# Optimization experiments

Hardware: AMD Instinct MI355X
Metric: run time of the kernel (lower is better)

The kernel has to match this reference:

```python
import jax, jax.numpy as jnp
import numpy as np

L = 3          # num_layers
H = 128        # hidden_dim
NH = 4         # num heads
DH = H // NH   # head dim
B = 32         # graphs per batch
N = 1024       # nodes per graph
NTOT = B * N
DEG = 16
E = NTOT * DEG
BN_EPS = 1e-5


def setup_inputs() -> dict:
    key = jax.random.key(0)
    ks = jax.random.split(key, 16)
    s = 1.0 / np.sqrt(H)
    inp = {
        "x": jax.random.normal(ks[0], (NTOT, H), jnp.float32),
        "edge_attr": jax.random.normal(ks[1], (E, H), jnp.float32),
        "gine_w1": jax.random.normal(ks[2], (L, H, H), jnp.float32) * s,
        "gine_b1": jnp.zeros((L, H), jnp.float32),
        "gine_bn_g": jnp.ones((L, H), jnp.float32),
        "gine_bn_b": jnp.zeros((L, H), jnp.float32),
        "gine_w2": jax.random.normal(ks[3], (L, H, H), jnp.float32) * s,
        "gine_b2": jnp.zeros((L, H), jnp.float32),
        "attn_wqkv": jax.random.normal(ks[4], (L, 3 * H, H), jnp.float32) * s,
        "attn_bqkv": jnp.zeros((L, 3 * H), jnp.float32),
        "attn_wo": jax.random.normal(ks[5], (L, H, H), jnp.float32) * s,
        "attn_bo": jnp.zeros((L, H), jnp.float32),
        "norm1_g": jnp.ones((L, H), jnp.float32),
        "norm1_b": jnp.zeros((L, H), jnp.float32),
        "norm2_g": jnp.ones((L, H), jnp.float32),
        "norm2_b": jnp.zeros((L, H), jnp.float32),
        "norm3_g": jnp.ones((L, H), jnp.float32),
        "norm3_b": jnp.zeros((L, H), jnp.float32),
        "mlp_w1": jax.random.normal(ks[6], (L, 2 * H, H), jnp.float32) * s,
        "mlp_b1": jnp.zeros((L, 2 * H), jnp.float32),
        "mlp_w2": jax.random.normal(ks[7], (L, H, 2 * H), jnp.float32) * (1.0 / np.sqrt(2 * H)),
        "mlp_b2": jnp.zeros((L, H), jnp.float32),
    }
    # intra-graph random edges: local src/dst in [0, N) plus per-graph offset
    offs = (jnp.arange(E, dtype=jnp.int32) // (N * DEG)) * N  # graph offset per edge
    src = jax.random.randint(ks[8], (E,), 0, N, jnp.int32) + offs
    dst = jax.random.randint(ks[9], (E,), 0, N, jnp.int32) + offs
    inp["edge_index"] = jnp.stack([src, dst]).astype(jnp.int32)
    inp["batch"] = (jnp.arange(NTOT, dtype=jnp.int32) // N)
    return inp


def _bn(x, g, b):
    m = x.mean(axis=0)
    v = jnp.var(x, axis=0)
    return (x - m) * jax.lax.rsqrt(v + BN_EPS) * g + b


def _gps_forward(x, edge_attr, gine_w1, gine_b1, gine_bn_g, gine_bn_b, gine_w2, gine_b2,
                 attn_wqkv, attn_bqkv, attn_wo, attn_bo,
                 norm1_g, norm1_b, norm2_g, norm2_b, norm3_g, norm3_b,
                 mlp_w1, mlp_b1, mlp_w2, mlp_b2, edge_index, batch):
    src, dst = edge_index[0], edge_index[1]
    for i in range(L):
        # ---- GINEConv: msg = relu(x_j + e), sum-scatter, nn-MLP on x + aggr (eps=0)
        msg = jax.nn.relu(x[src] + edge_attr)                       # [E, H]
        aggr = jax.ops.segment_sum(msg, dst, num_segments=NTOT)     # [NTOT, H]
        h = x + aggr
        h = h @ gine_w1[i].T + gine_b1[i]
        h = jax.nn.relu(_bn(h, gine_bn_g[i], gine_bn_b[i]))
        h = h @ gine_w2[i].T + gine_b2[i]
        h_local = _bn(h + x, norm1_g[i], norm1_b[i])                # residual + norm1
        # ---- global multi-head attention on x (dense per-graph, equal sizes)
        xb = x.reshape(B, N, H)
        qkv = xb @ attn_wqkv[i].T + attn_bqkv[i]                    # [B, N, 3H]
        q, k, v = jnp.split(qkv, 3, axis=-1)
        q = q.reshape(B, N, NH, DH).transpose(0, 2, 1, 3)           # [B, nh, N, dh]
        k = k.reshape(B, N, NH, DH).transpose(0, 2, 1, 3)
        v = v.reshape(B, N, NH, DH).transpose(0, 2, 1, 3)
        scores = jnp.einsum("bhqd,bhkd->bhqk", q, k) / np.sqrt(DH)
        attn = jax.nn.softmax(scores, axis=-1)
        o = jnp.einsum("bhqk,bhkd->bhqd", attn, v)
        o = o.transpose(0, 2, 1, 3).reshape(B, N, H) @ attn_wo[i].T + attn_bo[i]
        h_attn = _bn(o.reshape(NTOT, H) + x, norm2_g[i], norm2_b[i])
        # ---- combine + FFN + norm3
        out = h_local + h_attn
        ff = jax.nn.relu(out @ mlp_w1[i].T + mlp_b1[i]) @ mlp_w2[i].T + mlp_b2[i]
        x = _bn(out + ff, norm3_g[i], norm3_b[i])
        if i != L - 1:
            x = jax.nn.relu(x)
    return x


def reference(x, edge_attr, gine_w1, gine_b1, gine_bn_g, gine_bn_b, gine_w2, gine_b2,
              attn_wqkv, attn_bqkv, attn_wo, attn_bo,
              norm1_g, norm1_b, norm2_g, norm2_b, norm3_g, norm3_b,
              mlp_w1, mlp_b1, mlp_w2, mlp_b2, edge_index, batch):
    return _gps_forward(x, edge_attr, gine_w1, gine_b1, gine_bn_g, gine_bn_b, gine_w2, gine_b2,
                        attn_wqkv, attn_bqkv, attn_wo, attn_bo,
                        norm1_g, norm1_b, norm2_g, norm2_b, norm3_g, norm3_b,
                        mlp_w1, mlp_b1, mlp_w2, mlp_b2, edge_index, batch)
```

## Files before the change

kernel.cpp:

```cpp
#include <hip/hip_runtime.h>
#include <hip/hip_bf16.h>
#include <math.h>

#define NTOT 32768
#define HDIM 128
#define NE   524288
#define NGRAPH 32
#define NNODE 1024
#define NHEAD 4
#define DHEAD 32

typedef __attribute__((ext_vector_type(8))) short bf8v;
typedef __attribute__((ext_vector_type(4))) float f4v;

__device__ __forceinline__ float4 ld4(const float* p){ return *(const float4*)p; }

__device__ __forceinline__ unsigned short bf16rn(float f){
  union { float f; unsigned u; } x; x.f = f;
  unsigned r = x.u + 0x7FFF + ((x.u >> 16) & 1);
  return (unsigned short)(r >> 16);
}
__device__ __forceinline__ unsigned pk2(float a, float b){
  unsigned r;
  asm("v_cvt_pk_bf16_f32 %0, %1, %2" : "=v"(r) : "v"(a), "v"(b));
  return r;
}
__device__ __forceinline__ float bf2f(unsigned short u){
  union { unsigned u; float f; } x; x.u = ((unsigned)u) << 16;
  return x.f;
}

__global__ void k_count(const int* __restrict__ dst, int* __restrict__ deg){
  int e = blockIdx.x*256 + threadIdx.x;
  atomicAdd(&deg[dst[e]], 1);
}

__global__ __launch_bounds__(1024) void k_scan(const int* __restrict__ deg,
                                               int* __restrict__ indptr,
                                               int* __restrict__ cursor){
  __shared__ int sm[1024];
  int t = threadIdx.x;
  int base = t*32;
  int s = 0;
  for (int j=0;j<32;j++) s += deg[base+j];
  sm[t] = s; __syncthreads();
  for (int off=1; off<1024; off<<=1){
    int v = (t>=off) ? sm[t-off] : 0;
    __syncthreads();
    sm[t] += v;
    __syncthreads();
  }
  int ex = sm[t] - s;
  for (int j=0;j<32;j++){
    int d = deg[base+j];
    indptr[base+j] = ex; cursor[base+j] = ex;
    ex += d;
  }
  if (t == 1023) indptr[NTOT] = ex;
}

__global__ void k_fill(const int* __restrict__ dst, int* __restrict__ cursor,
                       int* __restrict__ perm){
  int e = blockIdx.x*256 + threadIdx.x;
  int pos = atomicAdd(&cursor[dst[e]], 1);
  perm[pos] = e;
}

__global__ __launch_bounds__(256) void k_eaprep(const float* __restrict__ ea,
    const int* __restrict__ src, const int* __restrict__ perm,
    unsigned short* __restrict__ EAb, int* __restrict__ SRCp){
  int tid = threadIdx.x;
  int p = blockIdx.x*8 + (tid>>5);
  int c4 = (tid&31)*4;
  int e = perm[p];
  float4 v = ld4(&ea[(size_t)e*HDIM + c4]);
  uint2 o; o.x = pk2(v.x, v.y); o.y = pk2(v.z, v.w);
  *(uint2*)&EAb[(size_t)p*HDIM + c4] = o;
  if ((tid&31) == 0) SRCp[p] = src[e];
}

__global__ __launch_bounds__(256) void k_aggr(const float* __restrict__ x,
                       const unsigned short* __restrict__ EAb,
                       const int* __restrict__ SRCp, const int* __restrict__ indptr,
                       float* __restrict__ aggr){
  int tid = threadIdx.x;
  int n = blockIdx.x*8 + (tid>>5);
  int c4 = (tid&31)*4;
  int p0 = indptr[n], p1 = indptr[n+1];
  float4 acc = make_float4(0.f,0.f,0.f,0.f);
  for (int p=p0;p<p1;p++){
    int s = SRCp[p];
    uint2 ev = *(const uint2*)&EAb[(size_t)p*HDIM + c4];
    float4 xv = ld4(&x[(size_t)s*HDIM + c4]);
    acc.x += fmaxf(xv.x + bf2f((unsigned short)(ev.x & 0xffff)), 0.f);
    acc.y += fmaxf(xv.y + bf2f((unsigned short)(ev.x >> 16)), 0.f);
    acc.z += fmaxf(xv.z + bf2f((unsigned short)(ev.y & 0xffff)), 0.f);
    acc.w += fmaxf(xv.w + bf2f((unsigned short)(ev.y >> 16)), 0.f);
  }
  *(float4*)&aggr[(size_t)n*HDIM + c4] = acc;
}

template<bool ADDA, bool BNA, bool RELU, bool EP, bool STATS>
__global__ __launch_bounds__(256) void k_gemm16(const float* __restrict__ A,
    const float* __restrict__ A2, const float* __restrict__ bnst,
    const float* __restrict__ W, const float* __restrict__ bias,
    const float* __restrict__ Ep, float* __restrict__ C, float* __restrict__ slot,
    int N, int K){
  __shared__ uint4 Asm[128*4];
  __shared__ uint4 Wsm[128*4];
  __shared__ float sred[256];
  int tid = threadIdx.x;
  int w = tid>>6, l = tid&63;
  int q = l&15, g = l>>4;
  int m0 = blockIdx.x*128, n0 = blockIdx.y*128;
  int wr = (w>>1)*64, wc = (w&1)*64;
  f4v acc[4][4];
  #pragma unroll
  for (int i=0;i<4;i++)
    #pragma unroll
    for (int j=0;j<4;j++) acc[i][j] = (f4v){0.f,0.f,0.f,0.f};
  int srow = tid & 127;
  int sgh  = tid >> 7;
  int sswz = (srow>>1)&3;

  for (int kc=0; kc<K; kc+=32){
    const float* pa = &A[(size_t)(m0+srow)*K + kc + sgh*16];
    float4 v0=ld4(pa), v1=ld4(pa+4), v2=ld4(pa+8), v3=ld4(pa+12);
    if (ADDA){
      const float* pb = &A2[(size_t)(m0+srow)*K + kc + sgh*16];
      float4 u0=ld4(pb), u1=ld4(pb+4), u2=ld4(pb+8), u3=ld4(pb+12);
      v0.x+=u0.x; v0.y+=u0.y; v0.z+=u0.z; v0.w+=u0.w;
      v1.x+=u1.x; v1.y+=u1.y; v1.z+=u1.z; v1.w+=u1.w;
      v2.x+=u2.x; v2.y+=u2.y; v2.z+=u2.z; v2.w+=u2.w;
      v3.x+=u3.x; v3.y+=u3.y; v3.z+=u3.z; v3.w+=u3.w;
    }
    if (BNA){
      int kb = kc + sgh*16;
      float4 s0=ld4(&bnst[256+kb]),  s1=ld4(&bnst[256+kb+4]);
      float4 s2=ld4(&bnst[256+kb+8]),s3=ld4(&bnst[256+kb+12]);
      float4 h0=ld4(&bnst[384+kb]),  h1=ld4(&bnst[384+kb+4]);
      float4 h2=ld4(&bnst[384+kb+8]),h3=ld4(&bnst[384+kb+12]);
      v0.x=fmaxf(v0.x*s0.x+h0.x,0.f); v0.y=fmaxf(v0.y*s0.y+h0.y,0.f);
      v0.z=fmaxf(v0.z*s0.z+h0.z,0.f); v0.w=fmaxf(v0.w*s0.w+h0.w,0.f);
      v1.x=fmaxf(v1.x*s1.x+h1.x,0.f); v1.y=fmaxf(v1.y*s1.y+h1.y,0.f);
      v1.z=fmaxf(v1.z*s1.z+h1.z,0.f); v1.w=fmaxf(v1.w*s1.w+h1.w,0.f);
      v2.x=fmaxf(v2.x*s2.x+h2.x,0.f); v2.y=fmaxf(v2.y*s2.y+h2.y,0.f);
      v2.z=fmaxf(v2.z*s2.z+h2.z,0.f); v2.w=fmaxf(v2.w*s2.w+h2.w,0.f);
      v3.x=fmaxf(v3.x*s3.x+h3.x,0.f); v3.y=fmaxf(v3.y*s3.y+h3.y,0.f);
      v3.z=fmaxf(v3.z*s3.z+h3.z,0.f); v3.w=fmaxf(v3.w*s3.w+h3.w,0.f);
    }
    uint4 ca, cb;
    ca.x=pk2(v0.x,v0.y); ca.y=pk2(v0.z,v0.w); ca.z=pk2(v1.x,v1.y); ca.w=pk2(v1.z,v1.w);
    cb.x=pk2(v2.x,v2.y); cb.y=pk2(v2.z,v2.w); cb.z=pk2(v3.x,v3.y); cb.w=pk2(v3.z,v3.w);
    const float* pw = &W[(size_t)(n0+srow)*K + kc + sgh*16];
    float4 w0=ld4(pw), w1=ld4(pw+4), w2=ld4(pw+8), w3=ld4(pw+12);
    uint4 da, db;
    da.x=pk2(w0.x,w0.y); da.y=pk2(w0.z,w0.w); da.z=pk2(w1.x,w1.y); da.w=pk2(w1.z,w1.w);
    db.x=pk2(w2.x,w2.y); db.y=pk2(w2.z,w2.w); db.z=pk2(w3.x,w3.y); db.w=pk2(w3.z,w3.w);
    __syncthreads();
    Asm[srow*4 + ((2*sgh  )^sswz)] = ca;
    Asm[srow*4 + ((2*sgh+1)^sswz)] = cb;
    Wsm[srow*4 + ((2*sgh  )^sswz)] = da;
    Wsm[srow*4 + ((2*sgh+1)^sswz)] = db;
    __syncthreads();
    bf8v af[4], bfv[4];
    #pragma unroll
    for (int mt=0;mt<4;mt++){
      int R = wr + 16*mt + q;
      af[mt] = *(const bf8v*)&Asm[R*4 + (g ^ ((R>>1)&3))];
    }
    #pragma unroll
    for (int nt=0;nt<4;nt++){
      int R = wc + 16*nt + q;
      bfv[nt] = *(const bf8v*)&Wsm[R*4 + (g ^ ((R>>1)&3))];
    }
    #pragma unroll
    for (int mt=0;mt<4;mt++)
      #pragma unroll
      for (int nt=0;nt<4;nt++)
        acc[mt][nt] = __builtin_amdgcn_mfma_f32_16x16x32_bf16(af[mt], bfv[nt], acc[mt][nt], 0,0,0);
  }
  float bbv[4];
  #pragma unroll
  for (int nt=0;nt<4;nt++) bbv[nt] = bias[n0 + wc + 16*nt + q];
  float csum[4] = {0.f,0.f,0.f,0.f}, csq[4] = {0.f,0.f,0.f,0.f};
  #pragma unroll
  for (int mt=0;mt<4;mt++){
    int row0 = m0 + wr + 16*mt + 4*g;
    #pragma unroll
    for (int nt=0;nt<4;nt++){
      int col = n0 + wc + 16*nt + q;
      #pragma unroll
      for (int r=0;r<4;r++){
        size_t off = (size_t)(row0+r)*N + col;
        float v = acc[mt][nt][r] + bbv[nt];
        if (EP) v += Ep[off];
        if (RELU) v = fmaxf(v, 0.f);
        C[off] = v;
        if (STATS){ csum[nt] += v; csq[nt] += v*v; }
      }
    }
  }
  if (STATS){
    if (tid < 128){ sred[tid] = 0.f; sred[128+tid] = 0.f; }
    __syncthreads();
    #pragma unroll
    for (int nt=0;nt<4;nt++){
      int col = wc + 16*nt + q;
      atomicAdd(&sred[col], csum[nt]);
      atomicAdd(&sred[128+col], csq[nt]);
    }
    __syncthreads();
    if (tid < 128){
      atomicAdd(&slot[tid], sred[tid]);
      atomicAdd(&slot[128+tid], sred[128+tid]);
    }
  }
}

__global__ __launch_bounds__(256) void k_gemmqkv(const float* __restrict__ A,
    const float* __restrict__ W, const float* __restrict__ bias,
    unsigned short* __restrict__ Qb, unsigned short* __restrict__ Kb,
    unsigned short* __restrict__ VT){
  __shared__ uint4 Asm[128*4];
  __shared__ uint4 Wsm[128*4];
  __shared__ unsigned short Sm[128*136];
  int tid = threadIdx.x;
  int w = tid>>6, l = tid&63;
  int q = l&15, g = l>>4;
  int which = blockIdx.y;
  int m0 = blockIdx.x*128, n0 = which*128;
  int wr = (w>>1)*64, wc = (w&1)*64;
  const int K = 128;
  f4v acc[4][4];
  #pragma unroll
  for (int i=0;i<4;i++)
    #pragma unroll
    for (int j=0;j<4;j++) acc[i][j] = (f4v){0.f,0.f,0.f,0.f};
  int srow = tid & 127;
  int sgh  = tid >> 7;
  int sswz = (srow>>1)&3;
  for (int kc=0; kc<K; kc+=32){
    const float* pa = &A[(size_t)(m0+srow)*K + kc + sgh*16];
    float4 v0=ld4(pa), v1=ld4(pa+4), v2=ld4(pa+8), v3=ld4(pa+12);
    uint4 ca, cb;
    ca.x=pk2(v0.x,v0.y); ca.y=pk2(v0.z,v0.w); ca.z=pk2(v1.x,v1.y); ca.w=pk2(v1.z,v1.w);
    cb.x=pk2(v2.x,v2.y); cb.y=pk2(v2.z,v2.w); cb.z=pk2(v3.x,v3.y); cb.w=pk2(v3.z,v3.w);
    const float* pw = &W[(size_t)(n0+srow)*K + kc + sgh*16];
    float4 w0=ld4(pw), w1=ld4(pw+4), w2=ld4(pw+8), w3=ld4(pw+12);
    uint4 da, db;
    da.x=pk2(w0.x,w0.y); da.y=pk2(w0.z,w0.w); da.z=pk2(w1.x,w1.y); da.w=pk2(w1.z,w1.w);
    db.x=pk2(w2.x,w2.y); db.y=pk2(w2.z,w2.w); db.z=pk2(w3.x,w3.y); db.w=pk2(w3.z,w3.w);
    __syncthreads();
    Asm[srow*4 + ((2*sgh  )^sswz)] = ca;
    Asm[srow*4 + ((2*sgh+1)^sswz)] = cb;
    Wsm[srow*4 + ((2*sgh  )^sswz)] = da;
    Wsm[srow*4 + ((2*sgh+1)^sswz)] = db;
    __syncthreads();
    bf8v af[4], bfv[4];
    #pragma unroll
    for (int mt=0;mt<4;mt++){
      int R = wr + 16*mt + q;
      af[mt] = *(const bf8v*)&Asm[R*4 + (g ^ ((R>>1)&3))];
    }
    #pragma unroll
    for (int nt=0;nt<4;nt++){
      int R = wc + 16*nt + q;
      bfv[nt] = *(const bf8v*)&Wsm[R*4 + (g ^ ((R>>1)&3))];
    }
    #pragma unroll
    for (int mt=0;mt<4;mt++)
      #pragma unroll
      for (int nt=0;nt<4;nt++)
        acc[mt][nt] = __builtin_amdgcn_mfma_f32_16x16x32_bf16(af[mt], bfv[nt], acc[mt][nt], 0,0,0);
  }
  const float QSC = 0.17677669529663687f * 1.4426950408889634f;
  float scale = (which==0) ? QSC : 1.0f;
  float bbv[4];
  #pragma unroll
  for (int nt=0;nt<4;nt++) bbv[nt] = bias[n0 + wc + 16*nt + q];
  __syncthreads();
  if (which < 2){
    #pragma unroll
    for (int mt=0;mt<4;mt++){
      int row0 = wr + 16*mt + 4*g;
      #pragma unroll
      for (int nt=0;nt<4;nt++){
        int col = wc + 16*nt + q;
        #pragma unroll
        for (int r=0;r<4;r++)
          Sm[(row0+r)*136 + col] = bf16rn((acc[mt][nt][r] + bbv[nt]) * scale);
      }
    }
    __syncthreads();
    unsigned short* dst = (which==0) ? Qb : Kb;
    #pragma unroll
    for (int it=0; it<8; it++){
      int idx = tid + it*256;
      int row = idx >> 4, c8 = (idx & 15) * 8;
      uint4 v = *(const uint4*)&Sm[row*136 + c8];
      *(uint4*)&dst[(size_t)(m0+row)*128 + c8] = v;
    }
  } else {
    #pragma unroll
    for (int mt=0;mt<4;mt++){
      int row0 = wr + 16*mt + 4*g;
      #pragma unroll
      for (int nt=0;nt<4;nt++){
        int col = wc + 16*nt + q;
        uint2 p;
        p.x = pk2(acc[mt][nt][0] + bbv[nt], acc[mt][nt][1] + bbv[nt]);
        p.y = pk2(acc[mt][nt][2] + bbv[nt], acc[mt][nt][3] + bbv[nt]);
        *(uint2*)&Sm[col*136 + row0] = p;
      }
    }
    __syncthreads();
    int gg = m0 >> 10;
    int nl0 = m0 - gg*1024;
    #pragma unroll
    for (int it=0; it<8; it++){
      int idx = tid + it*256;
      int c = idx >> 4, n8 = (idx & 15) * 8;
      uint4 v = *(const uint4*)&Sm[c*136 + n8];
      *(uint4*)&VT[((size_t)gg*128 + c)*1024 + nl0 + n8] = v;
    }
  }
}

__global__ __launch_bounds__(128) void k_bnfinal(const float* __restrict__ g, const float* __restrict__ b,
                                                 float* __restrict__ slot){
  int f = threadIdx.x;
  const float invn = 1.0f/32768.0f;
  float mean = slot[f]*invn;
  float var  = slot[128+f]*invn - mean*mean;
  float sc = g[f] * rsqrtf(var + 1e-5f);
  slot[256+f] = sc;
  slot[384+f] = b[f] - mean*sc;
}

template<bool RELU>
__global__ __launch_bounds__(256) void k_bnapply(const float* __restrict__ X,
                                                 const float* __restrict__ slot,
                                                 float* __restrict__ Y){
  size_t i = (size_t)blockIdx.x*256 + threadIdx.x;
  int c = (int)(i & 31) * 4;
  float4 v = ((const float4*)X)[i];
  float4 sc = *(const float4*)&slot[256+c];
  float4 sh = *(const float4*)&slot[384+c];
  float4 y;
  y.x = v.x*sc.x + sh.x; y.y = v.y*sc.y + sh.y;
  y.z = v.z*sc.z + sh.z; y.w = v.w*sc.w + sh.w;
  if (RELU){
    y.x=fmaxf(y.x,0.f); y.y=fmaxf(y.y,0.f); y.z=fmaxf(y.z,0.f); y.w=fmaxf(y.w,0.f);
  }
  ((float4*)Y)[i] = y;
}

__global__ __launch_bounds__(256) void k_add2bn(const float* __restrict__ A, const float* __restrict__ s1,
                                                const float* __restrict__ B, const float* __restrict__ s2,
                                                float* __restrict__ C){
  size_t i = (size_t)blockIdx.x*256 + threadIdx.x;
  int c = (int)(i & 31) * 4;
  float4 a = ((const float4*)A)[i];
  float4 b = ((const float4*)B)[i];
  float4 c1 = *(const float4*)&s1[256+c], d1 = *(const float4*)&s1[384+c];
  float4 c2 = *(const float4*)&s2[256+c], d2 = *(const float4*)&s2[384+c];
  float4 y;
  y.x = a.x*c1.x+d1.x + b.x*c2.x+d2.x;
  y.y = a.y*c1.y+d1.y + b.y*c2.y+d2.y;
  y.z = a.z*c1.z+d1.z + b.z*c2.z+d2.z;
  y.w = a.w*c1.w+d1.w + b.w*c2.w+d2.w;
  ((float4*)C)[i] = y;
}

__global__ __launch_bounds__(256) void k_flash2(const unsigned short* __restrict__ Qb,
    const unsigned short* __restrict__ Kb, const unsigned short* __restrict__ VT,
    float* __restrict__ O){
  __shared__ unsigned short Pl[4][16*72];
  int tid = threadIdx.x;
  int w = tid >> 6, l = tid & 63;
  int q = l & 15, grp = l >> 4;
  int qt = blockIdx.x, h = blockIdx.y, g = blockIdx.z;
  size_t gbase = (size_t)g*1024;
  size_t qrow0 = gbase + qt*64 + w*16;
  const unsigned short* Vp = VT + ((size_t)(g*4 + h)*32)*1024;
  bf8v qf = *(const bf8v*)&Qb[(qrow0 + q)*128 + h*32 + 8*grp];
  unsigned short* Pw = &Pl[w][0];
  float m = -1e30f, lsum = 0.f;
  f4v o0 = {0.f,0.f,0.f,0.f}, o1 = {0.f,0.f,0.f,0.f};
  for (int kt=0; kt<16; kt++){
    int k0 = kt*64;
    f4v st[4];
    #pragma unroll
    for (int t=0;t<4;t++){
      bf8v kf = *(const bf8v*)&Kb[(gbase + k0 + 16*t + q)*128 + h*32 + 8*grp];
      st[t] = __builtin_amdgcn_mfma_f32_16x16x32_bf16(kf, qf, (f4v){0.f,0.f,0.f,0.f}, 0,0,0);
    }
    float smax = st[0][0];
    #pragma unroll
    for (int t=0;t<4;t++)
      #pragma unroll
      for (int r=0;r<4;r++) smax = fmaxf(smax, st[t][r]);
    smax = fmaxf(smax, __shfl_xor(smax, 16));
    smax = fmaxf(smax, __shfl_xor(smax, 32));
    float mnew = fmaxf(m, smax);
    float alpha = exp2f(m - mnew);
    float psum = 0.f;
    #pragma unroll
    for (int t=0;t<4;t++){
      float p0 = exp2f(st[t][0]-mnew), p1 = exp2f(st[t][1]-mnew);
      float p2 = exp2f(st[t][2]-mnew), p3 = exp2f(st[t][3]-mnew);
      psum += (p0+p1)+(p2+p3);
      *(unsigned*)&Pw[q*72 + 16*t + 4*grp]     = pk2(p0,p1);
      *(unsigned*)&Pw[q*72 + 16*t + 4*grp + 2] = pk2(p2,p3);
    }
    psum += __shfl_xor(psum, 16);
    psum += __shfl_xor(psum, 32);
    lsum = lsum*alpha + psum;
    m = mnew;
    f4v aD;
    #pragma unroll
    for (int r=0;r<4;r++) aD[r] = __shfl(alpha, 4*grp + r);
    #pragma unroll
    for (int r=0;r<4;r++){ o0[r] *= aD[r]; o1[r] *= aD[r]; }
    bf8v pa0 = *(const bf8v*)&Pw[q*72 + 8*grp];
    bf8v pa1 = *(const bf8v*)&Pw[q*72 + 32 + 8*grp];
    bf8v v00 = *(const bf8v*)&Vp[(size_t)q*1024      + k0 + 8*grp];
    bf8v v01 = *(const bf8v*)&Vp[(size_t)q*1024      + k0 + 32 + 8*grp];
    bf8v v10 = *(const bf8v*)&Vp[(size_t)(16+q)*1024 + k0 + 8*grp];
    bf8v v11 = *(const bf8v*)&Vp[(size_t)(16+q)*1024 + k0 + 32 + 8*grp];
    o0 = __builtin_amdgcn_mfma_f32_16x16x32_bf16(pa0, v00, o0, 0,0,0);
    o0 = __builtin_amdgcn_mfma_f32_16x16x32_bf16(pa1, v01, o0, 0,0,0);
    o1 = __builtin_amdgcn_mfma_f32_16x16x32_bf16(pa0, v10, o1, 0,0,0);
    o1 = __builtin_amdgcn_mfma_f32_16x16x32_bf16(pa1, v11, o1, 0,0,0);
  }
  f4v lD;
  #pragma unroll
  for (int r=0;r<4;r++) lD[r] = __shfl(lsum, 4*grp + r);
  #pragma unroll
  for (int r=0;r<4;r++){
    float inv = 1.0f/lD[r];
    size_t row = qrow0 + 4*grp + r;
    O[row*HDIM + h*32 + q]      = o0[r]*inv;
    O[row*HDIM + h*32 + 16 + q] = o1[r]*inv;
  }
}

extern "C" void kernel_launch(void* const* d_in, const int* in_sizes, int n_in,
                              void* d_out, int out_size, void* d_ws, size_t ws_size,
                              hipStream_t stream){
  const float* x_in      = (const float*)d_in[0];
  const float* edge_attr = (const float*)d_in[1];
  const float* gine_w1   = (const float*)d_in[2];
  const float* gine_b1   = (const float*)d_in[3];
  const float* gine_bn_g = (const float*)d_in[4];
  const float* gine_bn_b = (const float*)d_in[5];
  const float* gine_w2   = (const float*)d_in[6];
  const float* gine_b2   = (const float*)d_in[7];
  const float* attn_wqkv = (const float*)d_in[8];
  const float* attn_bqkv = (const float*)d_in[9];
  const float* attn_wo   = (const float*)d_in[10];
  const float* attn_bo   = (const float*)d_in[11];
  const float* norm1_g   = (const float*)d_in[12];
  const float* norm1_b   = (const float*)d_in[13];
  const float* norm2_g   = (const float*)d_in[14];
  const float* norm2_b   = (const float*)d_in[15];
  const float* norm3_g   = (const float*)d_in[16];
  const float* norm3_b   = (const float*)d_in[17];
  const float* mlp_w1    = (const float*)d_in[18];
  const float* mlp_b1    = (const float*)d_in[19];
  const float* mlp_w2    = (const float*)d_in[20];
  const float* mlp_b2    = (const float*)d_in[21];
  const int* edge_index  = (const int*)d_in[22];
  const int* srcp = edge_index;
  const int* dstp = edge_index + NE;
  float* out = (float*)d_out;

  float* ws = (float*)d_ws;
  const size_t U = 4194304;
  float* X     = ws;
  float* AGGR  = ws + 1*U;
  float* H1    = ws + 2*U;
  float* H2    = ws + 3*U;
  float* OUT   = ws + 4*U;
  float* FF    = ws + 5*U;
  unsigned short* Qb  = (unsigned short*)(ws + 7*U);
  unsigned short* Kb  = Qb + (size_t)NTOT*128;
  unsigned short* VTb = Kb + (size_t)NTOT*128;
  float* STATS = ws + 10*U;
  int* IW      = (int*)(STATS + 12*512);
  int* deg     = IW;
  int* indptr  = IW + 32768;
  int* cursor  = IW + 32768 + 32772;
  int* perm    = cursor + 32768;
  unsigned short* EAb = (unsigned short*)(ws + 13*U);
  int* SRCp    = (int*)(ws + 21*U + U/2);

  hipMemsetAsync(STATS, 0, 12*512*sizeof(float), stream);
  hipMemsetAsync(deg, 0, NTOT*sizeof(int), stream);
  k_count<<<NE/256, 256, 0, stream>>>(dstp, deg);
  k_scan<<<1, 1024, 0, stream>>>(deg, indptr, cursor);
  k_fill<<<NE/256, 256, 0, stream>>>(dstp, cursor, perm);
  k_eaprep<<<NE/8, 256, 0, stream>>>(edge_attr, srcp, perm, EAb, SRCp);
  hipMemcpyAsync(X, x_in, (size_t)NTOT*HDIM*sizeof(float), hipMemcpyDeviceToDevice, stream);

  const int GAPPLY = (NTOT*HDIM/4)/256;
  dim3 gemmg1(NTOT/128, 1), gemmg2(NTOT/128, 2), gemmqkvg(NTOT/128, 3);

  for (int i=0;i<3;i++){
    const float* W1 = gine_w1 + (size_t)i*HDIM*HDIM;
    const float* B1 = gine_b1 + (size_t)i*HDIM;
    const float* W2 = gine_w2 + (size_t)i*HDIM*HDIM;
    const float* B2 = gine_b2 + (size_t)i*HDIM;
    const float* WQ = attn_wqkv + (size_t)i*3*HDIM*HDIM;
    const float* BQ = attn_bqkv + (size_t)i*3*HDIM;
    const float* WO = attn_wo + (size_t)i*HDIM*HDIM;
    const float* BO = attn_bo + (size_t)i*HDIM;
    const float* WM1 = mlp_w1 + (size_t)i*2*HDIM*HDIM;
    const float* BM1 = mlp_b1 + (size_t)i*2*HDIM;
    const float* WM2 = mlp_w2 + (size_t)i*2*HDIM*HDIM;
    const float* BM2 = mlp_b2 + (size_t)i*HDIM;
    float* S0 = STATS + (size_t)(i*4+0)*512;
    float* S1 = STATS + (size_t)(i*4+1)*512;
    float* S2 = STATS + (size_t)(i*4+2)*512;
    float* S3 = STATS + (size_t)(i*4+3)*512;

    k_aggr<<<NTOT/8, 256, 0, stream>>>(X, EAb, SRCp, indptr, AGGR);
    k_gemm16<true,false,false,false,true><<<gemmg1, 256, 0, stream>>>(X, AGGR, nullptr, W1, B1, nullptr, H1, S0, 128, 128);
    k_bnfinal<<<1, 128, 0, stream>>>(gine_bn_g + (size_t)i*HDIM, gine_bn_b + (size_t)i*HDIM, S0);
    k_gemm16<false,true,false,true,true><<<gemmg1, 256, 0, stream>>>(H1, nullptr, S0, W2, B2, X, AGGR, S1, 128, 128);
    k_bnfinal<<<1, 128, 0, stream>>>(norm1_g + (size_t)i*HDIM, norm1_b + (size_t)i*HDIM, S1);

    k_gemmqkv<<<gemmqkvg, 256, 0, stream>>>(X, WQ, BQ, Qb, Kb, VTb);
    k_flash2<<<dim3(16, NHEAD, NGRAPH), 256, 0, stream>>>(Qb, Kb, VTb, H1);
    k_gemm16<false,false,false,true,true><<<gemmg1, 256, 0, stream>>>(H1, nullptr, nullptr, WO, BO, X, H2, S2, 128, 128);
    k_bnfinal<<<1, 128, 0, stream>>>(norm2_g + (size_t)i*HDIM, norm2_b + (size_t)i*HDIM, S2);

    k_add2bn<<<GAPPLY, 256, 0, stream>>>(AGGR, S1, H2, S2, OUT);
    k_gemm16<false,false,true,false,false><<<gemmg2, 256, 0, stream>>>(OUT, nullptr, nullptr, WM1, BM1, nullptr, FF, nullptr, 256, 128);
    k_gemm16<false,false,false,true,true><<<gemmg1, 256, 0, stream>>>(FF, nullptr, nullptr, WM2, BM2, OUT, H2, S3, 128, 256);
    k_bnfinal<<<1, 128, 0, stream>>>(norm3_g + (size_t)i*HDIM, norm3_b + (size_t)i*HDIM, S3);
    float* dest = (i==2) ? out : X;
    if (i<2) k_bnapply<true ><<<GAPPLY, 256, 0, stream>>>(H2, S3, dest);
    else     k_bnapply<false><<<GAPPLY, 256, 0, stream>>>(H2, S3, dest);
  }
}
```

Before: 1.162 ms.

## Store activations and weights in bf16, drop LDS staging, fuse BN finalize into GEMMs

All intermediate activations (X, hidden, Q/K/V, FF, OUT) now live in bf16 instead of fp32, and weights are pre-converted to bf16 once per call. The GEMMs load MFMA fragments straight from global memory without LDS staging and use 128x64 tiles. BN finalize kernels are removed: scale and shift are computed in the consuming GEMM prologue or the apply kernel, and the add2bn pass is folded into the MLP1 GEMM. This cuts memory traffic and kernel launches, at the cost of extra bf16 rounding of residuals and BN inputs, plus uncoalesced direct global fragment loads.

```diff
diff --git a/kernel.cpp b/kernel.cpp
--- a/kernel.cpp
+++ b/kernel.cpp
@@ -12,20 +12,21 @@
 
 typedef __attribute__((ext_vector_type(8))) short bf8v;
 typedef __attribute__((ext_vector_type(4))) float f4v;
+typedef unsigned short u16;
 
 __device__ __forceinline__ float4 ld4(const float* p){ return *(const float4*)p; }
 
-__device__ __forceinline__ unsigned short bf16rn(float f){
+__device__ __forceinline__ u16 bf16rn(float f){
   union { float f; unsigned u; } x; x.f = f;
   unsigned r = x.u + 0x7FFF + ((x.u >> 16) & 1);
-  return (unsigned short)(r >> 16);
+  return (u16)(r >> 16);
 }
 __device__ __forceinline__ unsigned pk2(float a, float b){
   unsigned r;
   asm("v_cvt_pk_bf16_f32 %0, %1, %2" : "=v"(r) : "v"(a), "v"(b));
   return r;
 }
-__device__ __forceinline__ float bf2f(unsigned short u){
+__device__ __forceinline__ float bf2f(u16 u){
   union { unsigned u; float f; } x; x.u = ((unsigned)u) << 16;
   return x.f;
 }
@@ -68,7 +69,7 @@
 
 __global__ __launch_bounds__(256) void k_eaprep(const float* __restrict__ ea,
     const int* __restrict__ src, const int* __restrict__ perm,
-    unsigned short* __restrict__ EAb, int* __restrict__ SRCp){
+    u16* __restrict__ EAb, int* __restrict__ SRCp){
   int tid = threadIdx.x;
   int p = blockIdx.x*8 + (tid>>5);
   int c4 = (tid&31)*4;
@@ -79,197 +80,191 @@
   if ((tid&31) == 0) SRCp[p] = src[e];
 }
 
-__global__ __launch_bounds__(256) void k_aggr(const float* __restrict__ x,
-                       const unsigned short* __restrict__ EAb,
+__global__ __launch_bounds__(256) void k_xprep(const float* __restrict__ x, u16* __restrict__ Xb){
+  size_t i = ((size_t)blockIdx.x*256 + threadIdx.x)*4;
+  float4 v = ld4(&x[i]);
+  uint2 o; o.x = pk2(v.x,v.y); o.y = pk2(v.z,v.w);
+  *(uint2*)&Xb[i] = o;
+}
+
+__global__ __launch_bounds__(256) void k_wprep(const float* s0,const float* s1,const float* s2,
+    const float* s3,const float* s4,const float* s5, u16* __restrict__ Wb){
+  const float* srcs[6] = {s0,s1,s2,s3,s4,s5};
+  const int cnt4[6] = {12288,12288,36864,12288,24576,24576};
+  const int off[6]  = {0,49152,98304,245760,294912,393216};
+  int y = blockIdx.y;
+  int i = blockIdx.x*256 + threadIdx.x;
+  if (i >= cnt4[y]) return;
+  float4 v = ld4(&srcs[y][(size_t)i*4]);
+  uint2 o; o.x = pk2(v.x,v.y); o.y = pk2(v.z,v.w);
+  *(uint2*)&Wb[off[y] + (size_t)i*4] = o;
+}
+
+__global__ __launch_bounds__(256) void k_aggr(const u16* __restrict__ Xb,
+                       const u16* __restrict__ EAb,
                        const int* __restrict__ SRCp, const int* __restrict__ indptr,
-                       float* __restrict__ aggr){
+                       u16* __restrict__ Hb){
   int tid = threadIdx.x;
   int n = blockIdx.x*8 + (tid>>5);
   int c4 = (tid&31)*4;
   int p0 = indptr[n], p1 = indptr[n+1];
-  float4 acc = make_float4(0.f,0.f,0.f,0.f);
+  float a0=0.f,a1=0.f,a2=0.f,a3=0.f;
   for (int p=p0;p<p1;p++){
     int s = SRCp[p];
+    uint2 xv = *(const uint2*)&Xb[(size_t)s*HDIM + c4];
     uint2 ev = *(const uint2*)&EAb[(size_t)p*HDIM + c4];
-    float4 xv = ld4(&x[(size_t)s*HDIM + c4]);
-    acc.x += fmaxf(xv.x + bf2f((unsigned short)(ev.x & 0xffff)), 0.f);
-    acc.y += fmaxf(xv.y + bf2f((unsigned short)(ev.x >> 16)), 0.f);
-    acc.z += fmaxf(xv.z + bf2f((unsigned short)(ev.y & 0xffff)), 0.f);
-    acc.w += fmaxf(xv.w + bf2f((unsigned short)(ev.y >> 16)), 0.f);
-  }
-  *(float4*)&aggr[(size_t)n*HDIM + c4] = acc;
-}
-
-template<bool ADDA, bool BNA, bool RELU, bool EP, bool STATS>
-__global__ __launch_bounds__(256) void k_gemm16(const float* __restrict__ A,
-    const float* __restrict__ A2, const float* __restrict__ bnst,
-    const float* __restrict__ W, const float* __restrict__ bias,
-    const float* __restrict__ Ep, float* __restrict__ C, float* __restrict__ slot,
-    int N, int K){
-  __shared__ uint4 Asm[128*4];
-  __shared__ uint4 Wsm[128*4];
-  __shared__ float sred[256];
+    a0 += fmaxf(bf2f((u16)(xv.x&0xffff)) + bf2f((u16)(ev.x&0xffff)), 0.f);
+    a1 += fmaxf(bf2f((u16)(xv.x>>16))    + bf2f((u16)(ev.x>>16)), 0.f);
+    a2 += fmaxf(bf2f((u16)(xv.y&0xffff)) + bf2f((u16)(ev.y&0xffff)), 0.f);
+    a3 += fmaxf(bf2f((u16)(xv.y>>16))    + bf2f((u16)(ev.y>>16)), 0.f);
+  }
+  uint2 xn = *(const uint2*)&Xb[(size_t)n*HDIM + c4];
+  a0 += bf2f((u16)(xn.x&0xffff)); a1 += bf2f((u16)(xn.x>>16));
+  a2 += bf2f((u16)(xn.y&0xffff)); a3 += bf2f((u16)(xn.y>>16));
+  uint2 o; o.x = pk2(a0,a1); o.y = pk2(a2,a3);
+  *(uint2*)&Hb[(size_t)n*HDIM + c4] = o;
+}
+
+template<bool BNA, bool DUAL, bool RELU, bool EP, bool STATS, bool WROUT>
+__global__ __launch_bounds__(256) void k_bgemm(const u16* __restrict__ Ab,
+    const u16* __restrict__ A2b,
+    const float* __restrict__ slotA, const float* __restrict__ gA, const float* __restrict__ bA,
+    const float* __restrict__ slotB, const float* __restrict__ gB, const float* __restrict__ bB,
+    const u16* __restrict__ Wb, const float* __restrict__ bias,
+    const u16* __restrict__ Epb, u16* __restrict__ Cb,
+    u16* __restrict__ OUTb, float* __restrict__ slotOut, int N, int K){
+  __shared__ float sbnA[256];
+  __shared__ float sbnB[256];
+  __shared__ float sred[128];
   int tid = threadIdx.x;
   int w = tid>>6, l = tid&63;
   int q = l&15, g = l>>4;
-  int m0 = blockIdx.x*128, n0 = blockIdx.y*128;
-  int wr = (w>>1)*64, wc = (w&1)*64;
-  f4v acc[4][4];
-  #pragma unroll
-  for (int i=0;i<4;i++)
+  int m0 = blockIdx.x*128, n0 = blockIdx.y*64;
+  int wr = w*32;
+  const float invn = 1.0f/32768.0f;
+  if (BNA || DUAL){
+    if (tid < 128){
+      float mean = slotA[tid]*invn;
+      float var  = slotA[128+tid]*invn - mean*mean;
+      float sc = gA[tid] * rsqrtf(var + 1e-5f);
+      sbnA[tid] = sc; sbnA[128+tid] = bA[tid] - mean*sc;
+      if (DUAL){
+        float mean2 = slotB[tid]*invn;
+        float var2  = slotB[128+tid]*invn - mean2*mean2;
+        float sc2 = gB[tid] * rsqrtf(var2 + 1e-5f);
+        sbnB[tid] = sc2; sbnB[128+tid] = bB[tid] - mean2*sc2;
+      }
+    }
+  }
+  if (STATS && tid < 128) sred[tid] = 0.f;
+  if (BNA || DUAL || STATS) __syncthreads();
+
+  f4v acc[2][4];
+  #pragma unroll
+  for (int i=0;i<2;i++)
     #pragma unroll
     for (int j=0;j<4;j++) acc[i][j] = (f4v){0.f,0.f,0.f,0.f};
-  int srow = tid & 127;
-  int sgh  = tid >> 7;
-  int sswz = (srow>>1)&3;
 
   for (int kc=0; kc<K; kc+=32){
-    const float* pa = &A[(size_t)(m0+srow)*K + kc + sgh*16];
-    float4 v0=ld4(pa), v1=ld4(pa+4), v2=ld4(pa+8), v3=ld4(pa+12);
-    if (ADDA){
-      const float* pb = &A2[(size_t)(m0+srow)*K + kc + sgh*16];
-      float4 u0=ld4(pb), u1=ld4(pb+4), u2=ld4(pb+8), u3=ld4(pb+12);
-      v0.x+=u0.x; v0.y+=u0.y; v0.z+=u0.z; v0.w+=u0.w;
-      v1.x+=u1.x; v1.y+=u1.y; v1.z+=u1.z; v1.w+=u1.w;
-      v2.x+=u2.x; v2.y+=u2.y; v2.z+=u2.z; v2.w+=u2.w;
-      v3.x+=u3.x; v3.y+=u3.y; v3.z+=u3.z; v3.w+=u3.w;
-    }
-    if (BNA){
-      int kb = kc + sgh*16;
-      float4 s0=ld4(&bnst[256+kb]),  s1=ld4(&bnst[256+kb+4]);
-      float4 s2=ld4(&bnst[256+kb+8]),s3=ld4(&bnst[256+kb+12]);
-      float4 h0=ld4(&bnst[384+kb]),  h1=ld4(&bnst[384+kb+4]);
-      float4 h2=ld4(&bnst[384+kb+8]),h3=ld4(&bnst[384+kb+12]);
-      v0.x=fmaxf(v0.x*s0.x+h0.x,0.f); v0.y=fmaxf(v0.y*s0.y+h0.y,0.f);
-      v0.z=fmaxf(v0.z*s0.z+h0.z,0.f); v0.w=fmaxf(v0.w*s0.w+h0.w,0.f);
-      v1.x=fmaxf(v1.x*s1.x+h1.x,0.f); v1.y=fmaxf(v1.y*s1.y+h1.y,0.f);
-      v1.z=fmaxf(v1.z*s1.z+h1.z,0.f); v1.w=fmaxf(v1.w*s1.w+h1.w,0.f);
-      v2.x=fmaxf(v2.x*s2.x+h2.x,0.f); v2.y=fmaxf(v2.y*s2.y+h2.y,0.f);
-      v2.z=fmaxf(v2.z*s2.z+h2.z,0.f); v2.w=fmaxf(v2.w*s2.w+h2.w,0.f);
-      v3.x=fmaxf(v3.x*s3.x+h3.x,0.f); v3.y=fmaxf(v3.y*s3.y+h3.y,0.f);
-      v3.z=fmaxf(v3.z*s3.z+h3.z,0.f); v3.w=fmaxf(v3.w*s3.w+h3.w,0.f);
-    }
-    uint4 ca, cb;
-    ca.x=pk2(v0.x,v0.y); ca.y=pk2(v0.z,v0.w); ca.z=pk2(v1.x,v1.y); ca.w=pk2(v1.z,v1.w);
-    cb.x=pk2(v2.x,v2.y); cb.y=pk2(v2.z,v2.w); cb.z=pk2(v3.x,v3.y); cb.w=pk2(v3.z,v3.w);
-    const float* pw = &W[(size_t)(n0+srow)*K + kc + sgh*16];
-    float4 w0=ld4(pw), w1=ld4(pw+4), w2=ld4(pw+8), w3=ld4(pw+12);
-    uint4 da, db;
-    da.x=pk2(w0.x,w0.y); da.y=pk2(w0.z,w0.w); da.z=pk2(w1.x,w1.y); da.w=pk2(w1.z,w1.w);
-    db.x=pk2(w2.x,w2.y); db.y=pk2(w2.z,w2.w); db.z=pk2(w3.x,w3.y); db.w=pk2(w3.z,w3.w);
-    __syncthreads();
-    Asm[srow*4 + ((2*sgh  )^sswz)] = ca;
-    Asm[srow*4 + ((2*sgh+1)^sswz)] = cb;
-    Wsm[srow*4 + ((2*sgh  )^sswz)] = da;
-    Wsm[srow*4 + ((2*sgh+1)^sswz)] = db;
-    __syncthreads();
-    bf8v af[4], bfv[4];
-    #pragma unroll
-    for (int mt=0;mt<4;mt++){
-      int R = wr + 16*mt + q;
-      af[mt] = *(const bf8v*)&Asm[R*4 + (g ^ ((R>>1)&3))];
+    bf8v af[2], bfv[4];
+    #pragma unroll
+    for (int mt=0;mt<2;mt++){
+      int row = m0 + wr + 16*mt + q;
+      if (!BNA && !DUAL){
+        af[mt] = *(const bf8v*)&Ab[(size_t)row*K + kc + 8*g];
+      } else {
+        union { bf8v b; u16 s[8]; unsigned u[4]; } ra, r2, ro;
+        ra.b = *(const bf8v*)&Ab[(size_t)row*K + kc + 8*g];
+        if (DUAL) r2.b = *(const bf8v*)&A2b[(size_t)row*K + kc + 8*g];
+        float v[8];
+        #pragma unroll
+        for (int j=0;j<8;j++){
+          int kk = kc + 8*g + j;
+          float f = bf2f(ra.s[j]) * sbnA[kk] + sbnA[128+kk];
+          if (BNA) f = fmaxf(f, 0.f);
+          if (DUAL) f += bf2f(r2.s[j]) * sbnB[kk] + sbnB[128+kk];
+          v[j] = f;
+        }
+        ro.u[0]=pk2(v[0],v[1]); ro.u[1]=pk2(v[2],v[3]);
+        ro.u[2]=pk2(v[4],v[5]); ro.u[3]=pk2(v[6],v[7]);
+        af[mt] = ro.b;
+        if (WROUT && blockIdx.y == 0)
+          *(uint4*)&OUTb[(size_t)row*K + kc + 8*g] = *(uint4*)ro.u;
+      }
     }
     #pragma unroll
     for (int nt=0;nt<4;nt++){
-      int R = wc + 16*nt + q;
-      bfv[nt] = *(const bf8v*)&Wsm[R*4 + (g ^ ((R>>1)&3))];
-    }
-    #pragma unroll
-    for (int mt=0;mt<4;mt++)
+      int col = n0 + 16*nt + q;
+      bfv[nt] = *(const bf8v*)&Wb[(size_t)col*K + kc + 8*g];
+    }
+    #pragma unroll
+    for (int mt=0;mt<2;mt++)
       #pragma unroll
       for (int nt=0;nt<4;nt++)
         acc[mt][nt] = __builtin_amdgcn_mfma_f32_16x16x32_bf16(af[mt], bfv[nt], acc[mt][nt], 0,0,0);
   }
   float bbv[4];
   #pragma unroll
-  for (int nt=0;nt<4;nt++) bbv[nt] = bias[n0 + wc + 16*nt + q];
+  for (int nt=0;nt<4;nt++) bbv[nt] = bias[n0 + 16*nt + q];
   float csum[4] = {0.f,0.f,0.f,0.f}, csq[4] = {0.f,0.f,0.f,0.f};
   #pragma unroll
-  for (int mt=0;mt<4;mt++){
+  for (int mt=0;mt<2;mt++){
     int row0 = m0 + wr + 16*mt + 4*g;
     #pragma unroll
     for (int nt=0;nt<4;nt++){
-      int col = n0 + wc + 16*nt + q;
+      int col = n0 + 16*nt + q;
       #pragma unroll
       for (int r=0;r<4;r++){
         size_t off = (size_t)(row0+r)*N + col;
         float v = acc[mt][nt][r] + bbv[nt];
-        if (EP) v += Ep[off];
+        if (EP) v += bf2f(Epb[off]);
         if (RELU) v = fmaxf(v, 0.f);
-        C[off] = v;
+        Cb[off] = bf16rn(v);
         if (STATS){ csum[nt] += v; csq[nt] += v*v; }
       }
     }
   }
   if (STATS){
-    if (tid < 128){ sred[tid] = 0.f; sred[128+tid] = 0.f; }
+    #pragma unroll
+    for (int nt=0;nt<4;nt++){
+      int c = 16*nt + q;
+      atomicAdd(&sred[c], csum[nt]);
+      atomicAdd(&sred[64+c], csq[nt]);
+    }
     __syncthreads();
-    #pragma unroll
-    for (int nt=0;nt<4;nt++){
-      int col = wc + 16*nt + q;
-      atomicAdd(&sred[col], csum[nt]);
-      atomicAdd(&sred[128+col], csq[nt]);
-    }
-    __syncthreads();
-    if (tid < 128){
-      atomicAdd(&slot[tid], sred[tid]);
-      atomicAdd(&slot[128+tid], sred[128+tid]);
-    }
-  }
-}
-
-__global__ __launch_bounds__(256) void k_gemmqkv(const float* __restrict__ A,
-    const float* __restrict__ W, const float* __restrict__ bias,
-    unsigned short* __restrict__ Qb, unsigned short* __restrict__ Kb,
-    unsigned short* __restrict__ VT){
-  __shared__ uint4 Asm[128*4];
-  __shared__ uint4 Wsm[128*4];
-  __shared__ unsigned short Sm[128*136];
+    if (tid < 64){
+      atomicAdd(&slotOut[n0+tid], sred[tid]);
+      atomicAdd(&slotOut[128+n0+tid], sred[64+tid]);
+    }
+  }
+}
+
+__global__ __launch_bounds__(256) void k_qkvgemm(const u16* __restrict__ Ab,
+    const u16* __restrict__ Wb, const float* __restrict__ bias,
+    u16* __restrict__ Qb, u16* __restrict__ Kb, u16* __restrict__ VT){
+  __shared__ u16 Sm[128*72];
   int tid = threadIdx.x;
   int w = tid>>6, l = tid&63;
   int q = l&15, g = l>>4;
-  int which = blockIdx.y;
-  int m0 = blockIdx.x*128, n0 = which*128;
-  int wr = (w>>1)*64, wc = (w&1)*64;
+  int m0 = blockIdx.x*128, n0 = blockIdx.y*64;
+  int which = blockIdx.y >> 1, half = blockIdx.y & 1;
+  int wr = w*32;
   const int K = 128;
-  f4v acc[4][4];
-  #pragma unroll
-  for (int i=0;i<4;i++)
+  f4v acc[2][4];
+  #pragma unroll
+  for (int i=0;i<2;i++)
     #pragma unroll
     for (int j=0;j<4;j++) acc[i][j] = (f4v){0.f,0.f,0.f,0.f};
-  int srow = tid & 127;
-  int sgh  = tid >> 7;
-  int sswz = (srow>>1)&3;
   for (int kc=0; kc<K; kc+=32){
-    const float* pa = &A[(size_t)(m0+srow)*K + kc + sgh*16];
-    float4 v0=ld4(pa), v1=ld4(pa+4), v2=ld4(pa+8), v3=ld4(pa+12);
-    uint4 ca, cb;
-    ca.x=pk2(v0.x,v0.y); ca.y=pk2(v0.z,v0.w); ca.z=pk2(v1.x,v1.y); ca.w=pk2(v1.z,v1.w);
-    cb.x=pk2(v2.x,v2.y); cb.y=pk2(v2.z,v2.w); cb.z=pk2(v3.x,v3.y); cb.w=pk2(v3.z,v3.w);
-    const float* pw = &W[(size_t)(n0+srow)*K + kc + sgh*16];
-    float4 w0=ld4(pw), w1=ld4(pw+4), w2=ld4(pw+8), w3=ld4(pw+12);
-    uint4 da, db;
-    da.x=pk2(w0.x,w0.y); da.y=pk2(w0.z,w0.w); da.z=pk2(w1.x,w1.y); da.w=pk2(w1.z,w1.w);
-    db.x=pk2(w2.x,w2.y); db.y=pk2(w2.z,w2.w); db.z=pk2(w3.x,w3.y); db.w=pk2(w3.z,w3.w);
-    __syncthreads();
-    Asm[srow*4 + ((2*sgh  )^sswz)] = ca;
-    Asm[srow*4 + ((2*sgh+1)^sswz)] = cb;
-    Wsm[srow*4 + ((2*sgh  )^sswz)] = da;
-    Wsm[srow*4 + ((2*sgh+1)^sswz)] = db;
-    __syncthreads();
-    bf8v af[4], bfv[4];
-    #pragma unroll
-    for (int mt=0;mt<4;mt++){
-      int R = wr + 16*mt + q;
-      af[mt] = *(const bf8v*)&Asm[R*4 + (g ^ ((R>>1)&3))];
-    }
-    #pragma unroll
-    for (int nt=0;nt<4;nt++){
-      int R = wc + 16*nt + q;
-      bfv[nt] = *(const bf8v*)&Wsm[R*4 + (g ^ ((R>>1)&3))];
-    }
-    #pragma unroll
-    for (int mt=0;mt<4;mt++)
+    bf8v af[2], bfv[4];
+    #pragma unroll
+    for (int mt=0;mt<2;mt++)
+      af[mt] = *(const bf8v*)&Ab[(size_t)(m0+wr+16*mt+q)*K + kc + 8*g];
+    #pragma unroll
+    for (int nt=0;nt<4;nt++)
+      bfv[nt] = *(const bf8v*)&Wb[(size_t)(n0+16*nt+q)*K + kc + 8*g];
+    #pragma unroll
+    for (int mt=0;mt<2;mt++)
       #pragma unroll
       for (int nt=0;nt<4;nt++)
         acc[mt][nt] = __builtin_amdgcn_mfma_f32_16x16x32_bf16(af[mt], bfv[nt], acc[mt][nt], 0,0,0);
@@ -278,114 +273,100 @@
   float scale = (which==0) ? QSC : 1.0f;
   float bbv[4];
   #pragma unroll
-  for (int nt=0;nt<4;nt++) bbv[nt] = bias[n0 + wc + 16*nt + q];
-  __syncthreads();
+  for (int nt=0;nt<4;nt++) bbv[nt] = bias[n0 + 16*nt + q];
   if (which < 2){
     #pragma unroll
-    for (int mt=0;mt<4;mt++){
+    for (int mt=0;mt<2;mt++){
       int row0 = wr + 16*mt + 4*g;
       #pragma unroll
       for (int nt=0;nt<4;nt++){
-        int col = wc + 16*nt + q;
+        int c = 16*nt + q;
         #pragma unroll
         for (int r=0;r<4;r++)
-          Sm[(row0+r)*136 + col] = bf16rn((acc[mt][nt][r] + bbv[nt]) * scale);
+          Sm[(row0+r)*72 + c] = bf16rn((acc[mt][nt][r] + bbv[nt]) * scale);
       }
     }
     __syncthreads();
-    unsigned short* dst = (which==0) ? Qb : Kb;
-    #pragma unroll
-    for (int it=0; it<8; it++){
+    u16* dst = (which==0) ? Qb : Kb;
+    #pragma unroll
+    for (int it=0; it<4; it++){
       int idx = tid + it*256;
-      int row = idx >> 4, c8 = (idx & 15) * 8;
-      uint4 v = *(const uint4*)&Sm[row*136 + c8];
-      *(uint4*)&dst[(size_t)(m0+row)*128 + c8] = v;
+      int row = idx >> 3, c8 = (idx & 7) * 8;
+      uint4 v = *(const uint4*)&Sm[row*72 + c8];
+      *(uint4*)&dst[(size_t)(m0+row)*128 + half*64 + c8] = v;
     }
   } else {
     #pragma unroll
-    for (int mt=0;mt<4;mt++){
+    for (int mt=0;mt<2;mt++){
       int row0 = wr + 16*mt + 4*g;
       #pragma unroll
       for (int nt=0;nt<4;nt++){
-        int col = wc + 16*nt + q;
+        int c = 16*nt + q;
         uint2 p;
         p.x = pk2(acc[mt][nt][0] + bbv[nt], acc[mt][nt][1] + bbv[nt]);
         p.y = pk2(acc[mt][nt][2] + bbv[nt], acc[mt][nt][3] + bbv[nt]);
-        *(uint2*)&Sm[col*136 + row0] = p;
+        *(uint2*)&Sm[c*136 + row0] = p;
       }
     }
     __syncthreads();
     int gg = m0 >> 10;
     int nl0 = m0 - gg*1024;
     #pragma unroll
-    for (int it=0; it<8; it++){
+    for (int it=0; it<4; it++){
       int idx = tid + it*256;
       int c = idx >> 4, n8 = (idx & 15) * 8;
       uint4 v = *(const uint4*)&Sm[c*136 + n8];
-      *(uint4*)&VT[((size_t)gg*128 + c)*1024 + nl0 + n8] = v;
-    }
-  }
-}
-
-__global__ __launch_bounds__(128) void k_bnfinal(const float* __restrict__ g, const float* __restrict__ b,
-                                                 float* __restrict__ slot){
-  int f = threadIdx.x;
+      *(uint4*)&VT[((size_t)gg*128 + half*64 + c)*1024 + nl0 + n8] = v;
+    }
+  }
+}
+
+template<bool RELU, bool F32OUT>
+__global__ __launch_bounds__(256) void k_bnapply(const u16* __restrict__ X,
+    const float* __restrict__ slot, const float* __restrict__ gv, const float* __restrict__ bv,
+    u16* __restrict__ Yb, float* __restrict__ Yf){
+  int idx = blockIdx.x*256 + threadIdx.x;
+  int row = idx >> 4, c8 = (idx & 15) * 8;
   const float invn = 1.0f/32768.0f;
-  float mean = slot[f]*invn;
-  float var  = slot[128+f]*invn - mean*mean;
-  float sc = g[f] * rsqrtf(var + 1e-5f);
-  slot[256+f] = sc;
-  slot[384+f] = b[f] - mean*sc;
-}
-
-template<bool RELU>
-__global__ __launch_bounds__(256) void k_bnapply(const float* __restrict__ X,
-                                                 const float* __restrict__ slot,
-                                                 float* __restrict__ Y){
-  size_t i = (size_t)blockIdx.x*256 + threadIdx.x;
-  int c = (int)(i & 31) * 4;
-  float4 v = ((const float4*)X)[i];
-  float4 sc = *(const float4*)&slot[256+c];
-  float4 sh = *(const float4*)&slot[384+c];
-  float4 y;
-  y.x = v.x*sc.x + sh.x; y.y = v.y*sc.y + sh.y;
-  y.z = v.z*sc.z + sh.z; y.w = v.w*sc.w + sh.w;
-  if (RELU){
-    y.x=fmaxf(y.x,0.f); y.y=fmaxf(y.y,0.f); y.z=fmaxf(y.z,0.f); y.w=fmaxf(y.w,0.f);
-  }
-  ((float4*)Y)[i] = y;
-}
-
-__global__ __launch_bounds__(256) void k_add2bn(const float* __restrict__ A, const float* __restrict__ s1,
-                                                const float* __restrict__ B, const float* __restrict__ s2,
-                                                float* __restrict__ C){
-  size_t i = (size_t)blockIdx.x*256 + threadIdx.x;
-  int c = (int)(i & 31) * 4;
-  float4 a = ((const float4*)A)[i];
-  float4 b = ((const float4*)B)[i];
-  float4 c1 = *(const float4*)&s1[256+c], d1 = *(const float4*)&s1[384+c];
-  float4 c2 = *(const float4*)&s2[256+c], d2 = *(const float4*)&s2[384+c];
-  float4 y;
-  y.x = a.x*c1.x+d1.x + b.x*c2.x+d2.x;
-  y.y = a.y*c1.y+d1.y + b.y*c2.y+d2.y;
-  y.z = a.z*c1.z+d1.z + b.z*c2.z+d2.z;
-  y.w = a.w*c1.w+d1.w + b.w*c2.w+d2.w;
-  ((float4*)C)[i] = y;
-}
-
-__global__ __launch_bounds__(256) void k_flash2(const unsigned short* __restrict__ Qb,
-    const unsigned short* __restrict__ Kb, const unsigned short* __restrict__ VT,
-    float* __restrict__ O){
-  __shared__ unsigned short Pl[4][16*72];
+  union { uint4 u; u16 s[8]; } iv;
+  iv.u = *(const uint4*)&X[(size_t)row*HDIM + c8];
+  float o[8];
+  #pragma unroll
+  for (int j=0;j<8;j++){
+    int c = c8+j;
+    float mean = slot[c]*invn;
+    float var  = slot[128+c]*invn - mean*mean;
+    float sc = gv[c] * rsqrtf(var + 1e-5f);
+    float sh = bv[c] - mean*sc;
+    float v = bf2f(iv.s[j])*sc + sh;
+    if (RELU) v = fmaxf(v, 0.f);
+    o[j] = v;
+  }
+  if (F32OUT){
+    float* dst = &Yf[(size_t)row*HDIM + c8];
+    *(float4*)dst = make_float4(o[0],o[1],o[2],o[3]);
+    *(float4*)(dst+4) = make_float4(o[4],o[5],o[6],o[7]);
+  } else {
+    uint4 ov;
+    ov.x = pk2(o[0],o[1]); ov.y = pk2(o[2],o[3]);
+    ov.z = pk2(o[4],o[5]); ov.w = pk2(o[6],o[7]);
+    *(uint4*)&Yb[(size_t)row*HDIM + c8] = ov;
+  }
+}
+
+__global__ __launch_bounds__(256) void k_flash2(const u16* __restrict__ Qb,
+    const u16* __restrict__ Kb, const u16* __restrict__ VT,
+    u16* __restrict__ O){
+  __shared__ u16 Pl[4][16*72];
   int tid = threadIdx.x;
   int w = tid >> 6, l = tid & 63;
   int q = l & 15, grp = l >> 4;
   int qt = blockIdx.x, h = blockIdx.y, g = blockIdx.z;
   size_t gbase = (size_t)g*1024;
   size_t qrow0 = gbase + qt*64 + w*16;
-  const unsigned short* Vp = VT + ((size_t)(g*4 + h)*32)*1024;
+  const u16* Vp = VT + ((size_t)(g*4 + h)*32)*1024;
   bf8v qf = *(const bf8v*)&Qb[(qrow0 + q)*128 + h*32 + 8*grp];
-  unsigned short* Pw = &Pl[w][0];
+  u16* Pw = &Pl[w][0];
   float m = -1e30f, lsum = 0.f;
   f4v o0 = {0.f,0.f,0.f,0.f}, o1 = {0.f,0.f,0.f,0.f};
   for (int kt=0; kt<16; kt++){
@@ -441,8 +422,8 @@
   for (int r=0;r<4;r++){
     float inv = 1.0f/lD[r];
     size_t row = qrow0 + 4*grp + r;
-    O[row*HDIM + h*32 + q]      = o0[r]*inv;
-    O[row*HDIM + h*32 + 16 + q] = o1[r]*inv;
+    O[row*HDIM + h*32 + q]      = bf16rn(o0[r]*inv);
+    O[row*HDIM + h*32 + 16 + q] = bf16rn(o1[r]*inv);
   }
 }
 
@@ -478,23 +459,34 @@
 
   float* ws = (float*)d_ws;
   const size_t U = 4194304;
-  float* X     = ws;
-  float* AGGR  = ws + 1*U;
-  float* H1    = ws + 2*U;
-  float* H2    = ws + 3*U;
-  float* OUT   = ws + 4*U;
-  float* FF    = ws + 5*U;
-  unsigned short* Qb  = (unsigned short*)(ws + 7*U);
-  unsigned short* Kb  = Qb + (size_t)NTOT*128;
-  unsigned short* VTb = Kb + (size_t)NTOT*128;
-  float* STATS = ws + 10*U;
-  int* IW      = (int*)(STATS + 12*512);
+  u16* Xb   = (u16*)(ws);
+  u16* Hb   = (u16*)(ws + U/2);
+  u16* G1   = (u16*)(ws + U);
+  u16* P1   = (u16*)(ws + U + U/2);
+  u16* P2   = (u16*)(ws + 2*U);
+  u16* Ob   = (u16*)(ws + 2*U + U/2);
+  u16* FFb  = (u16*)(ws + 3*U);
+  u16* OUTb = (u16*)(ws + 4*U);
+  u16* H3   = (u16*)(ws + 4*U + U/2);
+  u16* Qb   = (u16*)(ws + 5*U);
+  u16* Kb   = (u16*)(ws + 5*U + U/2);
+  u16* VTb  = (u16*)(ws + 6*U);
+  u16* Wball= (u16*)(ws + 6*U + U/2);
+  float* STATS = ws + 7*U - 8192;
+  int* IW      = (int*)(ws + 7*U);
   int* deg     = IW;
   int* indptr  = IW + 32768;
   int* cursor  = IW + 32768 + 32772;
   int* perm    = cursor + 32768;
-  unsigned short* EAb = (unsigned short*)(ws + 13*U);
-  int* SRCp    = (int*)(ws + 21*U + U/2);
+  u16* EAb  = (u16*)(ws + 8*U);
+  int* SRCp = (int*)(ws + 16*U);
+
+  u16* W1b  = Wball + 0;
+  u16* W2b  = Wball + 49152;
+  u16* WQb  = Wball + 98304;
+  u16* WOb  = Wball + 245760;
+  u16* WM1b = Wball + 294912;
+  u16* WM2b = Wball + 393216;
 
   hipMemsetAsync(STATS, 0, 12*512*sizeof(float), stream);
   hipMemsetAsync(deg, 0, NTOT*sizeof(int), stream);
@@ -502,46 +494,56 @@
   k_scan<<<1, 1024, 0, stream>>>(deg, indptr, cursor);
   k_fill<<<NE/256, 256, 0, stream>>>(dstp, cursor, perm);
   k_eaprep<<<NE/8, 256, 0, stream>>>(edge_attr, srcp, perm, EAb, SRCp);
-  hipMemcpyAsync(X, x_in, (size_t)NTOT*HDIM*sizeof(float), hipMemcpyDeviceToDevice, stream);
-
-  const int GAPPLY = (NTOT*HDIM/4)/256;
-  dim3 gemmg1(NTOT/128, 1), gemmg2(NTOT/128, 2), gemmqkvg(NTOT/128, 3);
+  k_xprep<<<4096, 256, 0, stream>>>(x_in, Xb);
+  k_wprep<<<dim3(144,6), 256, 0, stream>>>(gine_w1, gine_w2, attn_wqkv, attn_wo, mlp_w1, mlp_w2, Wball);
+
+  dim3 gN128(NTOT/128, 2), gN256(NTOT/128, 4), gQKV(NTOT/128, 6);
 
   for (int i=0;i<3;i++){
-    const float* W1 = gine_w1 + (size_t)i*HDIM*HDIM;
     const float* B1 = gine_b1 + (size_t)i*HDIM;
-    const float* W2 = gine_w2 + (size_t)i*HDIM*HDIM;
     const float* B2 = gine_b2 + (size_t)i*HDIM;
-    const float* WQ = attn_wqkv + (size_t)i*3*HDIM*HDIM;
     const float* BQ = attn_bqkv + (size_t)i*3*HDIM;
-    const float* WO = attn_wo + (size_t)i*HDIM*HDIM;
     const float* BO = attn_bo + (size_t)i*HDIM;
-    const float* WM1 = mlp_w1 + (size_t)i*2*HDIM*HDIM;
     const float* BM1 = mlp_b1 + (size_t)i*2*HDIM;
-    const float* WM2 = mlp_w2 + (size_t)i*2*HDIM*HDIM;
     const float* BM2 = mlp_b2 + (size_t)i*HDIM;
+    u16* w1 = W1b + (size_t)i*16384;
+    u16* w2 = W2b + (size_t)i*16384;
+    u16* wq = WQb + (size_t)i*49152;
+    u16* wo = WOb + (size_t)i*16384;
+    u16* wm1 = WM1b + (size_t)i*32768;
+    u16* wm2 = WM2b + (size_t)i*32768;
     float* S0 = STATS + (size_t)(i*4+0)*512;
     float* S1 = STATS + (size_t)(i*4+1)*512;
     float* S2 = STATS + (size_t)(i*4+2)*512;
     float* S3 = STATS + (size_t)(i*4+3)*512;
-
-    k_aggr<<<NTOT/8, 256, 0, stream>>>(X, EAb, SRCp, indptr, AGGR);
-    k_gemm16<true,false,false,false,true><<<gemmg1, 256, 0, stream>>>(X, AGGR, nullptr, W1, B1, nullptr, H1, S0, 128, 128);
-    k_bnfinal<<<1, 128, 0, stream>>>(gine_bn_g + (size_t)i*HDIM, gine_bn_b + (size_t)i*HDIM, S0);
-    k_gemm16<false,true,false,true,true><<<gemmg1, 256, 0, stream>>>(H1, nullptr, S0, W2, B2, X, AGGR, S1, 128, 128);
-    k_bnfinal<<<1, 128, 0, stream>>>(norm1_g + (size_t)i*HDIM, norm1_b + (size_t)i*HDIM, S1);
-
-    k_gemmqkv<<<gemmqkvg, 256, 0, stream>>>(X, WQ, BQ, Qb, Kb, VTb);
-    k_flash2<<<dim3(16, NHEAD, NGRAPH), 256, 0, stream>>>(Qb, Kb, VTb, H1);
-    k_gemm16<false,false,false,true,true><<<gemmg1, 256, 0, stream>>>(H1, nullptr, nullptr, WO, BO, X, H2, S2, 128, 128);
-    k_bnfinal<<<1, 128, 0, stream>>>(norm2_g + (size_t)i*HDIM, norm2_b + (size_t)i*HDIM, S2);
-
-    k_add2bn<<<GAPPLY, 256, 0, stream>>>(AGGR, S1, H2, S2, OUT);
-    k_gemm16<false,false,true,false,false><<<gemmg2, 256, 0, stream>>>(OUT, nullptr, nullptr, WM1, BM1, nullptr, FF, nullptr, 256, 128);
-    k_gemm16<false,false,false,true,true><<<gemmg1, 256, 0, stream>>>(FF, nullptr, nullptr, WM2, BM2, OUT, H2, S3, 128, 256);
-    k_bnfinal<<<1, 128, 0, stream>>>(norm3_g + (size_t)i*HDIM, norm3_b + (size_t)i*HDIM, S3);
-    float* dest = (i==2) ? out : X;
-    if (i<2) k_bnapply<true ><<<GAPPLY, 256, 0, stream>>>(H2, S3, dest);
-    else     k_bnapply<false><<<GAPPLY, 256, 0, stream>>>(H2, S3, dest);
-  }
-}
+    const float* bnG = gine_bn_g + (size_t)i*HDIM;
+    const float* bnB = gine_bn_b + (size_t)i*HDIM;
+    const float* n1g = norm1_g + (size_t)i*HDIM, *n1b = norm1_b + (size_t)i*HDIM;
+    const float* n2g = norm2_g + (size_t)i*HDIM, *n2b = norm2_b + (size_t)i*HDIM;
+    const float* n3g = norm3_g + (size_t)i*HDIM, *n3b = norm3_b + (size_t)i*HDIM;
+
+    k_aggr<<<NTOT/8, 256, 0, stream>>>(Xb, EAb, SRCp, indptr, Hb);
+    k_bgemm<false,false,false,false,true,false><<<gN128, 256, 0, stream>>>(
+      Hb, nullptr, nullptr,nullptr,nullptr, nullptr,nullptr,nullptr,
+      w1, B1, nullptr, G1, nullptr, S0, 128, 128);
+    k_bgemm<true,false,false,true,true,false><<<gN128, 256, 0, stream>>>(
+      G1, nullptr, S0, bnG, bnB, nullptr,nullptr,nullptr,
+      w2, B2, Xb, P1, nullptr, S1, 128, 128);
+
+    k_qkvgemm<<<gQKV, 256, 0, stream>>>(Xb, wq, BQ, Qb, Kb, VTb);
+    k_flash2<<<dim3(16, NHEAD, NGRAPH), 256, 0, stream>>>(Qb, Kb, VTb, Ob);
+    k_bgemm<false,false,false,true,true,false><<<gN128, 256, 0, stream>>>(
+      Ob, nullptr, nullptr,nullptr,nullptr, nullptr,nullptr,nullptr,
+      wo, BO, Xb, P2, nullptr, S2, 128, 128);
+
+    k_bgemm<false,true,true,false,false,true><<<gN256, 256, 0, stream>>>(
+      P1, P2, S1, n1g, n1b, S2, n2g, n2b,
+      wm1, BM1, nullptr, FFb, OUTb, nullptr, 256, 128);
+    k_bgemm<false,false,false,true,true,false><<<gN128, 256, 0, stream>>>(
+      FFb, nullptr, nullptr,nullptr,nullptr, nullptr,nullptr,nullptr,
+      wm2, BM2, OUTb, H3, nullptr, S3, 128, 256);
+
+    if (i<2) k_bnapply<true ,false><<<2048, 256, 0, stream>>>(H3, S3, n3g, n3b, Xb, nullptr);
+    else     k_bnapply<false,true ><<<2048, 256, 0, stream>>>(H3, S3, n3g, n3b, nullptr, out);
+  }
+}
```

New measurement: 1.049 ms. 1.11x faster.
